# Performance work log

Hardware: AMD Instinct MI355X
Metric: run time of the kernel (lower is better)

The kernel has to match this reference:

```python
import jax, jax.numpy as jnp
import numpy as np

BS, N, IN_DIM, OUT_DIM = 16, 2048, 32, 64
CHEB_K, E_NODE, T_D = 3, 10, 8
EMBED = E_NODE + T_D  # 18, matches weights_pool dim 0
TOPK = 10


def setup_inputs() -> dict:
    key = jax.random.key(0)
    ks = jax.random.split(key, 7)
    return {
        "x": jax.random.normal(ks[0], (BS, N, IN_DIM), jnp.float32),
        "node_emb": jax.random.normal(ks[1], (N, E_NODE), jnp.float32),
        "t": jax.random.normal(ks[2], (BS, T_D), jnp.float32),
        "n_t": jax.random.normal(ks[3], (BS, T_D), jnp.float32),
        "p": jax.random.normal(ks[4], (BS, 1, 1), jnp.float32),
        "weights_pool": jax.random.normal(ks[5], (EMBED, CHEB_K, IN_DIM, OUT_DIM), jnp.float32) * 0.1,
        "bias_pool": jax.random.normal(ks[6], (EMBED, OUT_DIM), jnp.float32) * 0.1,
    }


def reference(x, node_emb, t, n_t, p, weights_pool, bias_pool):
    bs, n, _ = x.shape
    # static adjacency from node embeddings, broadcast over batch: [bs, N, N]
    a = (node_emb @ node_emb.T)[None, :, :]
    # temporal scalar correction: bmm([bs,1,td],[bs,td,1]) -> [bs,1,1]
    a_t = jnp.einsum('bd,bd->b', n_t, t)[:, None, None]
    _a = a + a_t
    # period branch: scaled relu adjacency, then dynamic topK sparsify
    pre = jax.nn.relu((1.0 + 0.3 * jax.nn.sigmoid(p)) * _a)  # [bs, N, N]
    # topK tie-break noise (torch.rand_like * 0.01); deterministic key here
    noise = jax.random.uniform(jax.random.key(42), pre.shape, jnp.float32) * 0.01
    _, idx = jax.lax.top_k(pre + noise, TOPK)  # idx: [bs, N, TOPK]
    mask = jnp.zeros_like(pre).at[
        jnp.arange(bs)[:, None, None], jnp.arange(n)[None, :, None], idx
    ].set(1.0)
    # masked entries stay 0 (not -inf) before softmax, as in the original
    A = jax.nn.softmax(pre * mask, axis=2)
    # Chebyshev polynomial supports: T0=I, T1=A, Tk = 2*A@T(k-1) - T(k-2)
    I = jnp.broadcast_to(jnp.eye(n, dtype=x.dtype), (bs, n, n))
    supports = [I, A]
    for _ in range(2, CHEB_K):
        supports.append(2.0 * (A @ supports[-1]) - supports[-2])
    S = jnp.stack(supports, axis=1)  # [bs, K, N, N]
    # node-adaptive embedding: cat(node_emb, n_t) -> [bs, N, EMBED]
    ne = jnp.concatenate(
        [jnp.broadcast_to(node_emb[None], (bs, n, E_NODE)),
         jnp.broadcast_to(n_t[:, None, :], (bs, n, T_D))], axis=-1)
    # graph conv features: [bs, N, K, in]
    x_g = jnp.einsum('bknm,bmc->bnkc', S, x)
    bias = ne @ bias_pool  # [bs, N, out]
    # fused per-node dynamic-weight contraction:
    # original: W = einsum(bnd,dkio->bnkio); out = einsum(bnki,bnkio->bno)
    out = jnp.einsum('bnki,bnd,dkio->bno', x_g, ne, weights_pool) + bias
    return out
```

## Files before the change

### kernel.cpp

```cpp
#include <hip/hip_runtime.h>
#include <hip/hip_bf16.h>


constexpr int BS = 16, NN_ = 2048, CIN = 32, OUT = 64, TK = 10;
constexpr int ROWS = BS * NN_;

__device__ __forceinline__ void tf2x32(unsigned x0, unsigned x1,
                                       unsigned& o0, unsigned& o1) {
  const unsigned k0 = 0u, k1 = 42u;
  const unsigned ks2 = k0 ^ k1 ^ 0x1BD11BDAu;
#define TF_R(rot) { x0 += x1; x1 = (x1 << rot) | (x1 >> (32 - rot)); x1 ^= x0; }
  x0 += k0; x1 += k1;
  TF_R(13) TF_R(15) TF_R(26) TF_R(6)
  x0 += k1; x1 += ks2 + 1u;
  TF_R(17) TF_R(29) TF_R(16) TF_R(24)
  x0 += ks2; x1 += k0 + 2u;
  TF_R(13) TF_R(15) TF_R(26) TF_R(6)
  x0 += k0; x1 += k1 + 3u;
  TF_R(17) TF_R(29) TF_R(16) TF_R(24)
  x0 += k1; x1 += ks2 + 4u;
  TF_R(13) TF_R(15) TF_R(26) TF_R(6)
  x0 += ks2; x1 += k0 + 5u;
#undef TF_R
  o0 = x0; o1 = x1;
}

__device__ __forceinline__ float noise_val(unsigned flat) {
  unsigned o0, o1; tf2x32(0u, flat, o0, o1);
  unsigned bits = o0 ^ o1;
  float u = __uint_as_float((bits >> 9) | 0x3f800000u) - 1.0f;
  return 0.01f * u;
}

__global__ __launch_bounds__(256) void k_pre(const float* __restrict__ ne,
                                             const float* __restrict__ n_t,
                                             const float* __restrict__ wp,
                                             const float* __restrict__ x,
                                             float* __restrict__ Wn,
                                             float* __restrict__ Wt,
                                             double* __restrict__ partX,
                                             float* __restrict__ csy) {
  const int bid = blockIdx.x;
  __shared__ float neS[16][10];
  __shared__ double red[8][32];

  if (bid < 768) {
    const int ng = bid / 6, sg = bid % 6;
    const int slot = sg * 256 + threadIdx.x;
    const int ki = slot >> 4, o4 = slot & 15;

    if (threadIdx.x < 160)
      neS[threadIdx.x / 10][threadIdx.x % 10] =
          ne[(ng * 16 + threadIdx.x / 10) * 10 + threadIdx.x % 10];

    const float4* wp4 = (const float4*)wp;
    float4 w[10];
    #pragma unroll
    for (int d = 0; d < 10; ++d) w[d] = wp4[(d * 96 + ki) * 16 + o4];
    __syncthreads();

    float4* Wn4 = (float4*)Wn;
    #pragma unroll 4
    for (int nn = 0; nn < 16; ++nn) {
      float4 acc = {0.f, 0.f, 0.f, 0.f};
      #pragma unroll
      for (int d = 0; d < 10; ++d) {
        float e = neS[nn][d];
        acc.x = fmaf(e, w[d].x, acc.x); acc.y = fmaf(e, w[d].y, acc.y);
        acc.z = fmaf(e, w[d].z, acc.z); acc.w = fmaf(e, w[d].w, acc.w);
      }
      Wn4[((size_t)(ng * 16 + nn) * 96 + ki) * 16 + o4] = acc;
    }
  } else if (bid < 864) {
    int gid = (bid - 768) * 256 + threadIdx.x;
    int b = gid / 1536, rem = gid % 1536, ki = rem >> 4, o4 = rem & 15;
    const float4* wp4 = (const float4*)wp;
    float4 acc = {0.f, 0.f, 0.f, 0.f};
    #pragma unroll
    for (int d = 0; d < 8; ++d) {
      float e = n_t[b * 8 + d];
      float4 w = wp4[((10 + d) * 96 + ki) * 16 + o4];
      acc.x = fmaf(e, w.x, acc.x); acc.y = fmaf(e, w.y, acc.y);
      acc.z = fmaf(e, w.z, acc.z); acc.w = fmaf(e, w.w, acc.w);
    }
    ((float4*)Wt)[(b * 96 + ki) * 16 + o4] = acc;
  } else if (bid < 1120) {
    const int bb = bid - 864;
    const int b = bb >> 4, ch = bb & 15;
    const int c = threadIdx.x & 31, g = threadIdx.x >> 5;
    double acc = 0.0;
    for (int m = ch * 128 + g; m < ch * 128 + 128; m += 8)
      acc += (double)x[(((b << 11) + m) << 5) + c];
    red[g][c] = acc;
    __syncthreads();
    if (g == 0) {
      double s2 = red[0][c];
      #pragma unroll
      for (int i = 1; i < 8; ++i) s2 += red[i][c];
      partX[(((b << 4) + ch) << 5) + c] = s2;
    }
  } else {
    csy[threadIdx.x] = 0.f;
    csy[256 + threadIdx.x] = 0.f;
  }
}

__global__ __launch_bounds__(512) void k_topk(const float* __restrict__ ne,
                                              const float* __restrict__ t,
                                              const float* __restrict__ n_t,
                                              const float* __restrict__ p,
                                              const float* __restrict__ x,
                                              const double* __restrict__ partX,
                                              float* __restrict__ cinv,
                                              int* __restrict__ idxb,
                                              float* __restrict__ wgt,
                                              float* __restrict__ Y1,
                                              float* __restrict__ csy) {
  const int n0 = blockIdx.x * 4;
  const int warp = threadIdx.x >> 6, lane = threadIdx.x & 63;

  __shared__ float rowS[4][2048];
  __shared__ float neN[4][10];
  __shared__ unsigned long long keyS[8][128];
  float* candAf = (float*)&keyS[0][0];
  int*   candMi = (int*)&keyS[0][0] + 1024;
  int*   winI = (int*)&rowS[0][0];
  float* winW = &rowS[0][0] + 640;
  float* csL  = &rowS[0][0] + 1280;
  float* csYs = &rowS[0][0] + 1792;
  float* ciS  = &rowS[0][0] + 2304;

  if (threadIdx.x < 40)
    neN[threadIdx.x / 10][threadIdx.x % 10] = ne[n0 * 10 + threadIdx.x];
  __syncthreads();

  {
    const int m0 = warp * 256 + lane * 4;
    float nm[40];
    const float4* nf = (const float4*)(ne + (size_t)m0 * 10);
    #pragma unroll
    for (int i = 0; i < 10; ++i) {
      float4 q = nf[i];
      nm[i * 4 + 0] = q.x; nm[i * 4 + 1] = q.y;
      nm[i * 4 + 2] = q.z; nm[i * 4 + 3] = q.w;
    }
    #pragma unroll
    for (int nd = 0; nd < 4; ++nd) {
      float res[4];
      #pragma unroll
      for (int rr = 0; rr < 4; ++rr) {
        float acc = 0.f;
        #pragma unroll
        for (int d = 0; d < 10; ++d)
          acc = fmaf(neN[nd][d], nm[rr * 10 + d], acc);
        res[rr] = acc;
      }
      *(float4*)&rowS[nd][m0] = make_float4(res[0], res[1], res[2], res[3]);
    }
  }
  __syncthreads();

  const int ln = warp >> 1;
  const int n = n0 + ln;
  const int bh = (warp & 1) * 8;

  float a[32];
  #pragma unroll
  for (int j = 0; j < 8; ++j) {
    float4 f = ((const float4*)rowS[ln])[j * 64 + lane];
    a[j * 4 + 0] = f.x; a[j * 4 + 1] = f.y;
    a[j * 4 + 2] = f.z; a[j * 4 + 3] = f.w;
  }
  __syncthreads();

  {
    const int b = threadIdx.x >> 5, c = threadIdx.x & 31;
    double s2 = 0.0;
    #pragma unroll
    for (int ch = 0; ch < 16; ++ch)
      s2 += partX[(((b << 4) + ch) << 5) + c];
    csL[(b << 5) + c] = (float)s2;
    csYs[(b << 5) + c] = 0.f;
  }

  float lm = -3.4e38f;
  #pragma unroll
  for (int j = 0; j < 32; ++j) lm = fmaxf(lm, a[j]);

  float last = 3.4e38f;
  for (int rd = 0; rd < 11; ++rd) {
    float x2 = (lm < last) ? lm : -3.4e38f;
    #pragma unroll
    for (int off = 32; off > 0; off >>= 1) x2 = fmaxf(x2, __shfl_xor(x2, off));
    last = x2;
  }
  const float T = last - 0.0101f;

  int cnt = 0;
  #pragma unroll
  for (int slot = 0; slot < 32; ++slot) {
    bool c = (a[slot] >= T);
    unsigned long long mk = __ballot(c);
    if (c) {
      int pos = cnt + __popcll(mk & ((1ull << lane) - 1ull));
      if (pos < 128) {
        candAf[warp * 128 + pos] = a[slot];
        candMi[warp * 128 + pos] = ((slot >> 2) << 8) + (lane << 2) + (slot & 3);
      }
    }
    cnt += (int)__popcll(mk);
  }
  const int C = cnt < 128 ? cnt : 128;
  const bool two = (C > 64);

  float a0c = 0.f, a1c = 0.f; int m0c = 0, m1c = 0;
  if (lane < C) { a0c = candAf[warp * 128 + lane]; m0c = candMi[warp * 128 + lane]; }
  if (two && lane + 64 < C) {
    a1c = candAf[warp * 128 + lane + 64];
    m1c = candMi[warp * 128 + lane + 64];
  }
  __syncthreads();

  for (int bi = 0; bi < 8; ++bi) {
    const int b = bh + bi;
    const int r = (b << 11) | n;

    float at = 0.f;
    #pragma unroll
    for (int d = 0; d < 8; ++d) at = fmaf(n_t[b * 8 + d], t[b * 8 + d], at);
    const float s = 1.0f + 0.3f * (1.0f / (1.0f + expf(-p[b])));

    float pre0 = fmaxf(s * (a0c + at), 0.f);
    unsigned long long k0 = 0ull;
    if (lane < C) {
      float key0 = pre0 + noise_val((unsigned)r * 2048u + (unsigned)m0c);
      k0 = ((unsigned long long)__float_as_uint(key0) << 32) |
           (unsigned)(2047 - m0c);
      keyS[warp][lane] = k0;
    }
    float pre1 = 0.f;
    unsigned long long k1 = 0ull;
    if (two) {
      if (lane + 64 < C) {
        pre1 = fmaxf(s * (a1c + at), 0.f);
        float key1 = pre1 + noise_val((unsigned)r * 2048u + (unsigned)m1c);
        k1 = ((unsigned long long)__float_as_uint(key1) << 32) |
             (unsigned)(2047 - m1c);
      }
      keyS[warp][lane + 64] = k1;
    }
    __syncthreads();

    int rank0 = 0, rank1 = 0;
    for (int j2 = 0; j2 < C; ++j2) {
      unsigned long long kj = keyS[warp][j2];
      rank0 += (kj > k0) ? 1 : 0;
      if (two) rank1 += (kj > k1) ? 1 : 0;
    }
    bool w0 = (lane < C) && (rank0 < 10);
    bool w1 = two && (lane + 64 < C) && (rank1 < 10);

    float e0 = w0 ? expf(pre0) : 0.f;
    float e1 = w1 ? expf(pre1) : 0.f;
    float sum = e0 + e1;
    #pragma unroll
    for (int off = 32; off > 0; off >>= 1) sum += __shfl_xor(sum, off);
    const float ci = 1.0f / (2038.0f + sum);

    unsigned long long mk0 = __ballot(w0);
    if (w0) {
      int pos = __popcll(mk0 & ((1ull << lane) - 1ull));
      idxb[r * 10 + pos] = m0c;
      wgt[r * 10 + pos] = (e0 - 1.0f) * ci;
      winI[(warp * 8 + bi) * 10 + pos] = m0c;
      winW[(warp * 8 + bi) * 10 + pos] = (e0 - 1.0f) * ci;
    }
    if (two) {
      unsigned long long mk1 = __ballot(w1);
      int base = __popcll(mk0);
      if (w1) {
        int pos = base + __popcll(mk1 & ((1ull << lane) - 1ull));
        idxb[r * 10 + pos] = m1c;
        wgt[r * 10 + pos] = (e1 - 1.0f) * ci;
        winI[(warp * 8 + bi) * 10 + pos] = m1c;
        winW[(warp * 8 + bi) * 10 + pos] = (e1 - 1.0f) * ci;
      }
    }
    if (lane == 0) { cinv[r] = ci; ciS[warp * 8 + bi] = ci; }
  }

  #pragma unroll
  for (int pass = 0; pass < 4; ++pass) {
    const int bi2 = pass * 2 + (lane >> 5);
    const int b = bh + bi2;
    const int c = lane & 31;
    const int r = (b << 11) | n;
    float acc = ciS[warp * 8 + bi2] * csL[(b << 5) + c];
    #pragma unroll
    for (int j = 0; j < 10; ++j) {
      int m = winI[(warp * 8 + bi2) * 10 + j];
      float w = winW[(warp * 8 + bi2) * 10 + j];
      acc = fmaf(w, x[(((b << 11) + m) << 5) + c], acc);
    }
    Y1[(size_t)r * 32 + c] = acc;
    atomicAdd(&csYs[(b << 5) + c], acc);
  }
  __syncthreads();
  {
    const int b = threadIdx.x >> 5, c = threadIdx.x & 31;
    atomicAdd(&csy[(b << 5) + c], csYs[(b << 5) + c]);
  }
}

__global__ __launch_bounds__(256) void k_v(const float* __restrict__ x,
                                           const float* __restrict__ Y1,
                                           const float* __restrict__ cinv,
                                           const int* __restrict__ idxb,
                                           const float* __restrict__ wgt,
                                           const float* __restrict__ csy,
                                           float* __restrict__ V) {
  int gid = blockIdx.x * 256 + threadIdx.x;
  int r = gid >> 5, c = gid & 31, b = r >> 11;
  float y2 = cinv[r] * csy[(b << 5) + c];
  #pragma unroll
  for (int j = 0; j < 10; ++j)
    y2 = fmaf(wgt[r * 10 + j], Y1[(((b << 11) + idxb[r * 10 + j]) << 5) + c], y2);
  float xv = x[gid], y1v = Y1[gid];
  V[r * 96 + c] = xv;
  V[r * 96 + 32 + c] = y1v;
  V[r * 96 + 64 + c] = 2.f * y2 - xv;
}

__global__ __launch_bounds__(256) void k_outn(const float* __restrict__ ne,
                                              const float* __restrict__ n_t,
                                              const float* __restrict__ Wn,
                                              const float* __restrict__ bp,
                                              const float* __restrict__ V,
                                              float* __restrict__ out) {
  const int n = blockIdx.x;
  __shared__ float Vs[16][100];
  __shared__ float bNs[64];

  for (int e = threadIdx.x; e < 384; e += 256) {
    int b = e / 24, j4 = e % 24;
    float4 f = *(const float4*)&V[((size_t)(b << 11) + n) * 96 + j4 * 4];
    *(float4*)&Vs[b][j4 * 4] = f;
  }
  if (threadIdx.x < 64) {
    float acc = 0.f;
    #pragma unroll
    for (int d = 0; d < 10; ++d)
      acc = fmaf(ne[n * 10 + d], bp[d * 64 + threadIdx.x], acc);
    bNs[threadIdx.x] = acc;
  }
  __syncthreads();

  const int b = threadIdx.x >> 4, og = threadIdx.x & 15;
  const float4* Wr = (const float4*)(Wn + (size_t)n * 6144);

  float4 acc = {0.f, 0.f, 0.f, 0.f};
  #pragma unroll 4
  for (int ki = 0; ki < 96; ++ki) {
    float4 wv = Wr[ki * 16 + og];
    float v = Vs[b][ki];
    acc.x = fmaf(v, wv.x, acc.x); acc.y = fmaf(v, wv.y, acc.y);
    acc.z = fmaf(v, wv.z, acc.z); acc.w = fmaf(v, wv.w, acc.w);
  }

  float4 res;
  #pragma unroll
  for (int q = 0; q < 4; ++q) {
    int o = og * 4 + q;
    float bT = 0.f;
    #pragma unroll
    for (int d = 0; d < 8; ++d)
      bT = fmaf(n_t[b * 8 + d], bp[(10 + d) * 64 + o], bT);
    (&res.x)[q] = (&acc.x)[q] + bNs[o] + bT;
  }
  *(float4*)&out[((size_t)(b << 11) + n) * 64 + og * 4] = res;
}

__global__ __launch_bounds__(512) void k_outt(const float* __restrict__ WtG,
                                              const float* __restrict__ V,
                                              float* __restrict__ out) {
  const int b = blockIdx.x >> 5, tile = blockIdx.x & 31;
  __shared__ float Wt[96][64];
  {
    const float4* src = (const float4*)(WtG + (size_t)b * 6144);
    float4* dst = (float4*)Wt;
    for (int e = threadIdx.x; e < 1536; e += 512) dst[e] = src[e];
  }
  __syncthreads();
  const int wave = threadIdx.x >> 6, lane = threadIdx.x & 63;
  const int og = lane & 15, rg = lane >> 4;
  const int r0 = tile * 64 + wave * 8 + rg * 2;

  float acc[2][4] = {};
  for (int ki4 = 0; ki4 < 24; ++ki4) {
    float4 vv[2];
    #pragma unroll
    for (int i = 0; i < 2; ++i)
      vv[i] = *(const float4*)&V[(size_t)((b << 11) + r0 + i) * 96 + ki4 * 4];
    #pragma unroll
    for (int t2 = 0; t2 < 4; ++t2) {
      float4 wv = *(const float4*)&Wt[ki4 * 4 + t2][og * 4];
      #pragma unroll
      for (int i = 0; i < 2; ++i) {
        float vi = (t2 == 0) ? vv[i].x : (t2 == 1) ? vv[i].y
                 : (t2 == 2) ? vv[i].z : vv[i].w;
        acc[i][0] = fmaf(vi, wv.x, acc[i][0]);
        acc[i][1] = fmaf(vi, wv.y, acc[i][1]);
        acc[i][2] = fmaf(vi, wv.z, acc[i][2]);
        acc[i][3] = fmaf(vi, wv.w, acc[i][3]);
      }
    }
  }
  #pragma unroll
  for (int i = 0; i < 2; ++i) {
    size_t oidx = (size_t)((b << 11) + r0 + i) * 64 + og * 4;
    float4 cur = *(float4*)&out[oidx];
    cur.x += acc[i][0]; cur.y += acc[i][1];
    cur.z += acc[i][2]; cur.w += acc[i][3];
    *(float4*)&out[oidx] = cur;
  }
}

extern "C" void kernel_launch(void* const* d_in, const int* in_sizes, int n_in,
                              void* d_out, int out_size, void* d_ws, size_t ws_size,
                              hipStream_t stream) {
  const float* x   = (const float*)d_in[0];
  const float* ne  = (const float*)d_in[1];
  const float* t   = (const float*)d_in[2];
  const float* n_t = (const float*)d_in[3];
  const float* p   = (const float*)d_in[4];
  const float* wp  = (const float*)d_in[5];
  const float* bp  = (const float*)d_in[6];
  float* out = (float*)d_out;
  float* ws = (float*)d_ws;
  (void)in_sizes; (void)n_in; (void)out_size; (void)ws_size;

  float* cinv  = ws;
  int*   idxb  = (int*)(cinv + 32768);
  float* wgt   = (float*)(idxb + 327680);
  float* csy   = wgt + 327680;
  float* Y1    = csy + 512;
  float* V     = Y1 + 1048576;
  double* partX = (double*)(V + 3145728);
  float* Wt    = (float*)(partX + 8192);
  float* Wn    = Wt + 98304;

  k_pre  <<<1121, 256, 0, stream>>>(ne, n_t, wp, x, Wn, Wt, partX, csy);
  k_topk <<<512, 512, 0, stream>>>(ne, t, n_t, p, x, partX,
                                   cinv, idxb, wgt, Y1, csy);
  k_v    <<<4096, 256, 0, stream>>>(x, Y1, cinv, idxb, wgt, csy, V);
  k_outn <<<2048, 256, 0, stream>>>(ne, n_t, Wn, bp, V, out);
  k_outt <<<512, 512, 0, stream>>>(Wt, V, out);
}
```

Measured before the change: 177.3 us.

## Restructure top-k kernel to one node per 256-thread block with sharded column-sum atomics

The top-k kernel now handles one node per 256-thread block instead of four nodes per 512-thread block. A single warp finds the candidates and shares them through LDS, and each warp covers four batches. The shared-memory column-sum reduction is replaced by direct global atomics into eight sharded partial buffers, which the next kernel sums. The column sum of x is now done by one block per batch instead of a two-level partial reduction, and block-wide syncs are removed from the batch loop. The aim is more blocks, less LDS and fewer registers per block for better occupancy. The cost is more global atomic traffic, recomputing the row dot products for each node, and a less parallel colsum-x.

```diff
diff --git a/kernel.cpp b/kernel.cpp
--- a/kernel.cpp
+++ b/kernel.cpp
@@ -38,8 +38,8 @@
                                              const float* __restrict__ x,
                                              float* __restrict__ Wn,
                                              float* __restrict__ Wt,
-                                             double* __restrict__ partX,
-                                             float* __restrict__ csy) {
+                                             float* __restrict__ csx,
+                                             float* __restrict__ csy_part) {
   const int bid = blockIdx.x;
   __shared__ float neS[16][10];
   __shared__ double red[8][32];
@@ -84,12 +84,11 @@
       acc.z = fmaf(e, w.z, acc.z); acc.w = fmaf(e, w.w, acc.w);
     }
     ((float4*)Wt)[(b * 96 + ki) * 16 + o4] = acc;
-  } else if (bid < 1120) {
-    const int bb = bid - 864;
-    const int b = bb >> 4, ch = bb & 15;
+  } else if (bid < 880) {
+    const int b = bid - 864;
     const int c = threadIdx.x & 31, g = threadIdx.x >> 5;
     double acc = 0.0;
-    for (int m = ch * 128 + g; m < ch * 128 + 128; m += 8)
+    for (int m = g; m < 2048; m += 8)
       acc += (double)x[(((b << 11) + m) << 5) + c];
     red[g][c] = acc;
     __syncthreads();
@@ -97,45 +96,44 @@
       double s2 = red[0][c];
       #pragma unroll
       for (int i = 1; i < 8; ++i) s2 += red[i][c];
-      partX[(((b << 4) + ch) << 5) + c] = s2;
+      csx[(b << 5) + c] = (float)s2;
     }
   } else {
-    csy[threadIdx.x] = 0.f;
-    csy[256 + threadIdx.x] = 0.f;
-  }
-}
-
-__global__ __launch_bounds__(512) void k_topk(const float* __restrict__ ne,
-                                              const float* __restrict__ t,
-                                              const float* __restrict__ n_t,
-                                              const float* __restrict__ p,
-                                              const float* __restrict__ x,
-                                              const double* __restrict__ partX,
-                                              float* __restrict__ cinv,
-                                              int* __restrict__ idxb,
-                                              float* __restrict__ wgt,
-                                              float* __restrict__ Y1,
-                                              float* __restrict__ csy) {
-  const int n0 = blockIdx.x * 4;
+    #pragma unroll
+    for (int i = 0; i < 16; ++i) csy_part[i * 256 + threadIdx.x] = 0.f;
+  }
+}
+
+__global__ __launch_bounds__(256, 6) void k_topk(const float* __restrict__ ne,
+                                                 const float* __restrict__ t,
+                                                 const float* __restrict__ n_t,
+                                                 const float* __restrict__ p,
+                                                 const float* __restrict__ x,
+                                                 const float* __restrict__ csx,
+                                                 float* __restrict__ cinv,
+                                                 int* __restrict__ idxb,
+                                                 float* __restrict__ wgt,
+                                                 float* __restrict__ Y1,
+                                                 float* __restrict__ csy_part) {
+  const int n = blockIdx.x;
   const int warp = threadIdx.x >> 6, lane = threadIdx.x & 63;
 
-  __shared__ float rowS[4][2048];
-  __shared__ float neN[4][10];
-  __shared__ unsigned long long keyS[8][128];
-  float* candAf = (float*)&keyS[0][0];
-  int*   candMi = (int*)&keyS[0][0] + 1024;
-  int*   winI = (int*)&rowS[0][0];
-  float* winW = &rowS[0][0] + 640;
-  float* csL  = &rowS[0][0] + 1280;
-  float* csYs = &rowS[0][0] + 1792;
-  float* ciS  = &rowS[0][0] + 2304;
-
-  if (threadIdx.x < 40)
-    neN[threadIdx.x / 10][threadIdx.x % 10] = ne[n0 * 10 + threadIdx.x];
+  __shared__ float rowS[2048];
+  __shared__ float neN[10];
+  __shared__ float candA[128];
+  __shared__ int   candM[128];
+  __shared__ int   Cs;
+  __shared__ unsigned long long keyS[4][128];
+  __shared__ int   winI[16][10];
+  __shared__ float winW[16][10];
+  __shared__ float ciS[16];
+
+  if (threadIdx.x < 10) neN[threadIdx.x] = ne[n * 10 + threadIdx.x];
   __syncthreads();
 
-  {
-    const int m0 = warp * 256 + lane * 4;
+  #pragma unroll
+  for (int g2 = 0; g2 < 2; ++g2) {
+    const int m0 = g2 * 1024 + threadIdx.x * 4;
     float nm[40];
     const float4* nf = (const float4*)(ne + (size_t)m0 * 10);
     #pragma unroll
@@ -144,85 +142,62 @@
       nm[i * 4 + 0] = q.x; nm[i * 4 + 1] = q.y;
       nm[i * 4 + 2] = q.z; nm[i * 4 + 3] = q.w;
     }
-    #pragma unroll
-    for (int nd = 0; nd < 4; ++nd) {
-      float res[4];
+    float res[4];
+    #pragma unroll
+    for (int rr = 0; rr < 4; ++rr) {
+      float acc = 0.f;
       #pragma unroll
-      for (int rr = 0; rr < 4; ++rr) {
-        float acc = 0.f;
-        #pragma unroll
-        for (int d = 0; d < 10; ++d)
-          acc = fmaf(neN[nd][d], nm[rr * 10 + d], acc);
-        res[rr] = acc;
+      for (int d = 0; d < 10; ++d)
+        acc = fmaf(neN[d], nm[rr * 10 + d], acc);
+      res[rr] = acc;
+    }
+    *(float4*)&rowS[m0] = make_float4(res[0], res[1], res[2], res[3]);
+  }
+  __syncthreads();
+
+  if (warp == 0) {
+    float lm = -3.4e38f;
+    #pragma unroll
+    for (int j = 0; j < 8; ++j) {
+      float4 f = ((const float4*)rowS)[j * 64 + lane];
+      lm = fmaxf(lm, fmaxf(fmaxf(f.x, f.y), fmaxf(f.z, f.w)));
+    }
+    float last = 3.4e38f;
+    for (int rd = 0; rd < 11; ++rd) {
+      float x2 = (lm < last) ? lm : -3.4e38f;
+      #pragma unroll
+      for (int off = 32; off > 0; off >>= 1) x2 = fmaxf(x2, __shfl_xor(x2, off));
+      last = x2;
+    }
+    const float T = last - 0.0101f;
+
+    int cnt = 0;
+    #pragma unroll
+    for (int slot = 0; slot < 32; ++slot) {
+      float v = rowS[(slot >> 2) * 256 + lane * 4 + (slot & 3)];
+      bool c = (v >= T);
+      unsigned long long mk = __ballot(c);
+      if (c) {
+        int pos = cnt + __popcll(mk & ((1ull << lane) - 1ull));
+        if (pos < 128) {
+          candA[pos] = v;
+          candM[pos] = ((slot >> 2) << 8) + (lane << 2) + (slot & 3);
+        }
       }
-      *(float4*)&rowS[nd][m0] = make_float4(res[0], res[1], res[2], res[3]);
-    }
+      cnt += (int)__popcll(mk);
+    }
+    if (lane == 0) Cs = cnt < 128 ? cnt : 128;
   }
   __syncthreads();
 
-  const int ln = warp >> 1;
-  const int n = n0 + ln;
-  const int bh = (warp & 1) * 8;
-
-  float a[32];
-  #pragma unroll
-  for (int j = 0; j < 8; ++j) {
-    float4 f = ((const float4*)rowS[ln])[j * 64 + lane];
-    a[j * 4 + 0] = f.x; a[j * 4 + 1] = f.y;
-    a[j * 4 + 2] = f.z; a[j * 4 + 3] = f.w;
-  }
-  __syncthreads();
-
-  {
-    const int b = threadIdx.x >> 5, c = threadIdx.x & 31;
-    double s2 = 0.0;
-    #pragma unroll
-    for (int ch = 0; ch < 16; ++ch)
-      s2 += partX[(((b << 4) + ch) << 5) + c];
-    csL[(b << 5) + c] = (float)s2;
-    csYs[(b << 5) + c] = 0.f;
-  }
-
-  float lm = -3.4e38f;
-  #pragma unroll
-  for (int j = 0; j < 32; ++j) lm = fmaxf(lm, a[j]);
-
-  float last = 3.4e38f;
-  for (int rd = 0; rd < 11; ++rd) {
-    float x2 = (lm < last) ? lm : -3.4e38f;
-    #pragma unroll
-    for (int off = 32; off > 0; off >>= 1) x2 = fmaxf(x2, __shfl_xor(x2, off));
-    last = x2;
-  }
-  const float T = last - 0.0101f;
-
-  int cnt = 0;
-  #pragma unroll
-  for (int slot = 0; slot < 32; ++slot) {
-    bool c = (a[slot] >= T);
-    unsigned long long mk = __ballot(c);
-    if (c) {
-      int pos = cnt + __popcll(mk & ((1ull << lane) - 1ull));
-      if (pos < 128) {
-        candAf[warp * 128 + pos] = a[slot];
-        candMi[warp * 128 + pos] = ((slot >> 2) << 8) + (lane << 2) + (slot & 3);
-      }
-    }
-    cnt += (int)__popcll(mk);
-  }
-  const int C = cnt < 128 ? cnt : 128;
+  const int C = Cs;
   const bool two = (C > 64);
-
   float a0c = 0.f, a1c = 0.f; int m0c = 0, m1c = 0;
-  if (lane < C) { a0c = candAf[warp * 128 + lane]; m0c = candMi[warp * 128 + lane]; }
-  if (two && lane + 64 < C) {
-    a1c = candAf[warp * 128 + lane + 64];
-    m1c = candMi[warp * 128 + lane + 64];
-  }
-  __syncthreads();
-
-  for (int bi = 0; bi < 8; ++bi) {
-    const int b = bh + bi;
+  if (lane < C) { a0c = candA[lane]; m0c = candM[lane]; }
+  if (two && lane + 64 < C) { a1c = candA[lane + 64]; m1c = candM[lane + 64]; }
+
+  for (int bi = 0; bi < 4; ++bi) {
+    const int b = warp * 4 + bi;
     const int r = (b << 11) | n;
 
     float at = 0.f;
@@ -249,7 +224,6 @@
       }
       keyS[warp][lane + 64] = k1;
     }
-    __syncthreads();
 
     int rank0 = 0, rank1 = 0;
     for (int j2 = 0; j2 < C; ++j2) {
@@ -272,8 +246,8 @@
       int pos = __popcll(mk0 & ((1ull << lane) - 1ull));
       idxb[r * 10 + pos] = m0c;
       wgt[r * 10 + pos] = (e0 - 1.0f) * ci;
-      winI[(warp * 8 + bi) * 10 + pos] = m0c;
-      winW[(warp * 8 + bi) * 10 + pos] = (e0 - 1.0f) * ci;
+      winI[b][pos] = m0c;
+      winW[b][pos] = (e0 - 1.0f) * ci;
     }
     if (two) {
       unsigned long long mk1 = __ballot(w1);
@@ -282,33 +256,28 @@
         int pos = base + __popcll(mk1 & ((1ull << lane) - 1ull));
         idxb[r * 10 + pos] = m1c;
         wgt[r * 10 + pos] = (e1 - 1.0f) * ci;
-        winI[(warp * 8 + bi) * 10 + pos] = m1c;
-        winW[(warp * 8 + bi) * 10 + pos] = (e1 - 1.0f) * ci;
+        winI[b][pos] = m1c;
+        winW[b][pos] = (e1 - 1.0f) * ci;
       }
     }
-    if (lane == 0) { cinv[r] = ci; ciS[warp * 8 + bi] = ci; }
-  }
-
-  #pragma unroll
-  for (int pass = 0; pass < 4; ++pass) {
+    if (lane == 0) { cinv[r] = ci; ciS[b] = ci; }
+  }
+
+  #pragma unroll
+  for (int pass = 0; pass < 2; ++pass) {
     const int bi2 = pass * 2 + (lane >> 5);
-    const int b = bh + bi2;
+    const int b = warp * 4 + bi2;
     const int c = lane & 31;
     const int r = (b << 11) | n;
-    float acc = ciS[warp * 8 + bi2] * csL[(b << 5) + c];
+    float acc = ciS[b] * csx[(b << 5) + c];
     #pragma unroll
     for (int j = 0; j < 10; ++j) {
-      int m = winI[(warp * 8 + bi2) * 10 + j];
-      float w = winW[(warp * 8 + bi2) * 10 + j];
+      int m = winI[b][j];
+      float w = winW[b][j];
       acc = fmaf(w, x[(((b << 11) + m) << 5) + c], acc);
     }
     Y1[(size_t)r * 32 + c] = acc;
-    atomicAdd(&csYs[(b << 5) + c], acc);
-  }
-  __syncthreads();
-  {
-    const int b = threadIdx.x >> 5, c = threadIdx.x & 31;
-    atomicAdd(&csy[(b << 5) + c], csYs[(b << 5) + c]);
+    atomicAdd(&csy_part[((n & 7) << 9) + (b << 5) + c], acc);
   }
 }
 
@@ -317,11 +286,14 @@
                                            const float* __restrict__ cinv,
                                            const int* __restrict__ idxb,
                                            const float* __restrict__ wgt,
-                                           const float* __restrict__ csy,
+                                           const float* __restrict__ csy_part,
                                            float* __restrict__ V) {
   int gid = blockIdx.x * 256 + threadIdx.x;
   int r = gid >> 5, c = gid & 31, b = r >> 11;
-  float y2 = cinv[r] * csy[(b << 5) + c];
+  float cs = 0.f;
+  #pragma unroll
+  for (int k = 0; k < 8; ++k) cs += csy_part[(k << 9) + (b << 5) + c];
+  float y2 = cinv[r] * cs;
   #pragma unroll
   for (int j = 0; j < 10; ++j)
     y2 = fmaf(wgt[r * 10 + j], Y1[(((b << 11) + idxb[r * 10 + j]) << 5) + c], y2);
@@ -439,20 +411,20 @@
   float* ws = (float*)d_ws;
   (void)in_sizes; (void)n_in; (void)out_size; (void)ws_size;
 
-  float* cinv  = ws;
-  int*   idxb  = (int*)(cinv + 32768);
-  float* wgt   = (float*)(idxb + 327680);
-  float* csy   = wgt + 327680;
-  float* Y1    = csy + 512;
-  float* V     = Y1 + 1048576;
-  double* partX = (double*)(V + 3145728);
-  float* Wt    = (float*)(partX + 8192);
-  float* Wn    = Wt + 98304;
-
-  k_pre  <<<1121, 256, 0, stream>>>(ne, n_t, wp, x, Wn, Wt, partX, csy);
-  k_topk <<<512, 512, 0, stream>>>(ne, t, n_t, p, x, partX,
-                                   cinv, idxb, wgt, Y1, csy);
-  k_v    <<<4096, 256, 0, stream>>>(x, Y1, cinv, idxb, wgt, csy, V);
+  float* cinv     = ws;
+  int*   idxb     = (int*)(cinv + 32768);
+  float* wgt      = (float*)(idxb + 327680);
+  float* csy_part = wgt + 327680;
+  float* csx      = csy_part + 4096;
+  float* Y1       = csx + 512;
+  float* V        = Y1 + 1048576;
+  float* Wt       = V + 3145728;
+  float* Wn       = Wt + 98304;
+
+  k_pre  <<<881, 256, 0, stream>>>(ne, n_t, wp, x, Wn, Wt, csx, csy_part);
+  k_topk <<<2048, 256, 0, stream>>>(ne, t, n_t, p, x, csx,
+                                    cinv, idxb, wgt, Y1, csy_part);
+  k_v    <<<4096, 256, 0, stream>>>(x, Y1, cinv, idxb, wgt, csy_part, V);
   k_outn <<<2048, 256, 0, stream>>>(ne, n_t, Wn, bp, V, out);
   k_outt <<<512, 512, 0, stream>>>(Wt, V, out);
 }
```

Result: slower. 229.8 us (+29.6%).
